# Kernel optimization log

Measured on AMD Instinct MI355X. Metric: run time of the kernel, lower is better.

The kernel has to match this reference:

```python
import jax, jax.numpy as jnp
import numpy as np

B, L, D, H = 2, 2048, 1024, 16
HD = D // H  # head_dim = 64


def _clin(xr, xi, Wr, br, Wi, bi):
    # (x_r + i x_i)(W_r + i W_i): out_r = fc_r(x_r) - fc_i(x_i); out_i = fc_r(x_i) + fc_i(x_r)
    rr = xr @ Wr.T + br
    ii = xi @ Wi.T + bi
    ri = xi @ Wr.T + br
    ir = xr @ Wi.T + bi
    return rr - ii, ri + ir


def _heads(x):
    # [B, L, D] -> [B, H, L, HD]
    return x.reshape(B, L, H, HD).transpose(0, 2, 1, 3)


def setup_inputs() -> dict:
    key = jax.random.key(0)
    ks = jax.random.split(key, 11)
    inp = {
        "x_r": jax.random.normal(ks[0], (B, L, D), jnp.float32),
        "x_i": jax.random.normal(ks[1], (B, L, D), jnp.float32),
        "attention_mask": jnp.zeros((B, 1, 1, L), jnp.float32),
    }
    names = ["Wq_r", "Wq_i", "Wk_r", "Wk_i", "Wv_r", "Wv_i", "Wo_r", "Wo_i"]
    for n, k in zip(names, ks[2:10]):
        inp[n] = jax.random.normal(k, (D, D), jnp.float32) * 0.02
        inp["b" + n[1:]] = jnp.zeros((D,), jnp.float32)
    return inp


def reference(x_r, x_i, attention_mask,
              Wq_r, bq_r, Wq_i, bq_i,
              Wk_r, bk_r, Wk_i, bk_i,
              Wv_r, bv_r, Wv_i, bv_i,
              Wo_r, bo_r, Wo_i, bo_i):
    qr, qi = _clin(x_r, x_i, Wq_r, bq_r, Wq_i, bq_i)
    kr, ki = _clin(x_r, x_i, Wk_r, bk_r, Wk_i, bk_i)
    vr, vi = _clin(x_r, x_i, Wv_r, bv_r, Wv_i, bv_i)
    q_r, q_i = _heads(qr), _heads(qi)
    k_r, k_i = _heads(kr), _heads(ki)
    v_r, v_i = _heads(vr), _heads(vi)
    # complex QK^T cross terms -> squared-magnitude interference score
    s_real = jnp.einsum('bhqd,bhkd->bhqk', q_r, k_r) + jnp.einsum('bhqd,bhkd->bhqk', q_i, k_i)
    s_imag = jnp.einsum('bhqd,bhkd->bhqk', q_i, k_r) - jnp.einsum('bhqd,bhkd->bhqk', q_r, k_i)
    interference = (s_real * s_real + s_imag * s_imag) / HD + attention_mask
    attn = jax.nn.softmax(interference, axis=-1)
    c_r = jnp.einsum('bhqk,bhkd->bhqd', attn, v_r).transpose(0, 2, 1, 3).reshape(B, L, D)
    c_i = jnp.einsum('bhqk,bhkd->bhqd', attn, v_i).transpose(0, 2, 1, 3).reshape(B, L, D)
    out_r, out_i = _clin(c_r, c_i, Wo_r, bo_r, Wo_i, bo_i)
    return out_r, out_i
```

## Files before the change

### kernel.cpp

```cpp
#include <hip/hip_runtime.h>
#include <hip/hip_bf16.h>

typedef unsigned short u16;
typedef __attribute__((ext_vector_type(8))) short bf16x8;
typedef __attribute__((ext_vector_type(8))) _Float16 f16x8;
typedef __attribute__((ext_vector_type(2))) _Float16 f16x2;
typedef __attribute__((ext_vector_type(8))) unsigned short u16x8;
typedef __attribute__((ext_vector_type(4))) float f32x4;
typedef __attribute__((ext_vector_type(16))) float f32x16;

__device__ __forceinline__ u16 f2b(float f) {
  _Float16 h = (_Float16)f;
  return __builtin_bit_cast(u16, h);
}

__device__ __forceinline__ f32x4 mfma16(bf16x8 a, bf16x8 b, f32x4 c) {
  return __builtin_amdgcn_mfma_f32_16x16x32_f16(
      __builtin_bit_cast(f16x8, a), __builtin_bit_cast(f16x8, b), c, 0, 0, 0);
}

__device__ __forceinline__ f32x16 mfma32(bf16x8 a, bf16x8 b, f32x16 c) {
  return __builtin_amdgcn_mfma_f32_32x32x16_f16(
      __builtin_bit_cast(f16x8, a), __builtin_bit_cast(f16x8, b), c, 0, 0, 0);
}

__device__ __forceinline__ float fexp2(float x) {
  float r; asm("v_exp_f32 %0, %1" : "=v"(r) : "v"(x)); return r;
}

#define GLD16(dst, src) __builtin_amdgcn_global_load_lds( \
    (const __attribute__((address_space(1))) void*)(src), \
    (__attribute__((address_space(3))) void*)(dst), 16, 0, 0)

__global__ void pack_x_kernel(u16* __restrict__ A1, const float* __restrict__ xr,
                              const float* __restrict__ xi) {
  const int id = blockIdx.x * 256 + threadIdx.x;
  const size_t k8 = (size_t)id * 8;
  const int n = (int)(k8 >> 11);
  const int kk = (int)(k8 & 2047);
  const float* src = (kk < 1024) ? (xr + (size_t)n * 1024 + kk)
                                 : (xi + (size_t)n * 1024 + (kk - 1024));
  float4 a = *(const float4*)src;
  float4 c = *(const float4*)(src + 4);
  u16x8 o;
  o[0] = f2b(a.x); o[1] = f2b(a.y); o[2] = f2b(a.z); o[3] = f2b(a.w);
  o[4] = f2b(c.x); o[5] = f2b(c.y); o[6] = f2b(c.z); o[7] = f2b(c.w);
  *(u16x8*)(A1 + k8) = o;
}

struct PWArgs {
  const float* Wr[4]; const float* Wi[4];
  const float* br[4]; const float* bi[4];
};

__global__ void pack_w_all(PWArgs a, int sbase, u16* __restrict__ B1,
                           u16* __restrict__ B2, float* __restrict__ bias1,
                           float* __restrict__ bias2) {
  const int s = sbase + blockIdx.y;
  const int wi = s >> 1, isim = s & 1;
  u16* dst = (s < 6) ? (B1 + (size_t)s * (1024 * 2048))
                     : (B2 + (size_t)(s - 6) * (1024 * 2048));
  float* biasDst = (s < 6) ? (bias1 + s * 1024) : (bias2 + (s - 6) * 1024);
  const int row = blockIdx.x;
  const int kk = threadIdx.x * 8;
  const int half = kk >> 10;
  const int kloc = kk & 1023;
  const float* W = (half == 0) ? (isim ? a.Wi[wi] : a.Wr[wi])
                               : (isim ? a.Wr[wi] : a.Wi[wi]);
  const float sgn = (half == 1 && !isim) ? -1.f : 1.f;
  const float* src = W + (size_t)row * 1024 + kloc;
  float4 x = *(const float4*)src;
  float4 c = *(const float4*)(src + 4);
  u16x8 o;
  o[0] = f2b(sgn * x.x); o[1] = f2b(sgn * x.y); o[2] = f2b(sgn * x.z); o[3] = f2b(sgn * x.w);
  o[4] = f2b(sgn * c.x); o[5] = f2b(sgn * c.y); o[6] = f2b(sgn * c.z); o[7] = f2b(sgn * c.w);
  *(u16x8*)(dst + (size_t)row * 2048 + kk) = o;
  if (threadIdx.x == 0)
    biasDst[row] = isim ? (a.br[wi][row] + a.bi[wi][row])
                        : (a.br[wi][row] - a.bi[wi][row]);
}

template<int MODE>
__global__ __launch_bounds__(256) void gemm_bt(const u16* __restrict__ A,
                                               const u16* __restrict__ Bw,
                                               const float* __restrict__ bias,
                                               void* __restrict__ outp,
                                               u16* __restrict__ vtp) {
  constexpr int K = 2048;
  __shared__ __align__(16) u16 As[128 * 64];
  __shared__ __align__(16) u16 Bs[128 * 64];
  const int tid = threadIdx.x;
  const int w = tid >> 6, l = tid & 63;
  const int l15 = l & 15, lhi = l >> 4;
  const int m0 = blockIdx.y * 128, n0 = blockIdx.x * 128;
  const int wm = w >> 1, wn = w & 1;
  f32x4 acc[4][4] = {};
  for (int kt = 0; kt < K; kt += 64) {
#pragma unroll
    for (int it = 0; it < 4; ++it) {
      const int grp = it * 4 + w;
      const int cl = grp * 64 + l;
      const int r = cl >> 3;
      const int g = (cl & 7) ^ (r & 7);
      GLD16(As + grp * 512, A + (size_t)(m0 + r) * K + kt + g * 8);
      GLD16(Bs + grp * 512, Bw + (size_t)(n0 + r) * K + kt + g * 8);
    }
    __syncthreads();
#pragma unroll
    for (int ks = 0; ks < 2; ++ks) {
      const int c = ks * 4 + lhi;
      bf16x8 af[4], bfr[4];
#pragma unroll
      for (int mf = 0; mf < 4; ++mf) {
        const int r = wm * 64 + mf * 16 + l15;
        af[mf] = *(const bf16x8*)&As[r * 64 + ((c ^ (r & 7)) << 3)];
      }
#pragma unroll
      for (int nf = 0; nf < 4; ++nf) {
        const int r = wn * 64 + nf * 16 + l15;
        bfr[nf] = *(const bf16x8*)&Bs[r * 64 + ((c ^ (r & 7)) << 3)];
      }
#pragma unroll
      for (int mf = 0; mf < 4; ++mf)
#pragma unroll
        for (int nf = 0; nf < 4; ++nf)
          acc[mf][nf] = mfma16(af[mf], bfr[nf], acc[mf][nf]);
    }
    __syncthreads();
  }
#pragma unroll
  for (int nf = 0; nf < 4; ++nf) {
    const int j = n0 + wn * 64 + nf * 16 + l15;
    const float bv = bias[j];
    if constexpr (MODE == 1) {
      const size_t obase = (size_t)(j >> 10) * (4096 * 1024) + (j & 1023);
#pragma unroll
      for (int mf = 0; mf < 4; ++mf)
#pragma unroll
        for (int i = 0; i < 4; ++i) {
          const int row = m0 + wm * 64 + mf * 16 + lhi * 4 + i;
          ((float*)outp)[obase + (size_t)row * 1024] = acc[mf][nf][i] + bv;
        }
    } else {
      if (j < 4096) {
        const size_t obase = (size_t)(j >> 10) * (4096 * 1024) + (j & 1023);
#pragma unroll
        for (int mf = 0; mf < 4; ++mf)
#pragma unroll
          for (int i = 0; i < 4; ++i) {
            const int row = m0 + wm * 64 + mf * 16 + lhi * 4 + i;
            ((u16*)outp)[obase + (size_t)row * 1024] = f2b(acc[mf][nf][i] + bv);
          }
      } else {
        const int jv = j - 4096;
        const size_t vb = (size_t)(jv >> 10) * 4194304 +
                          (size_t)((jv >> 6) & 15) * 131072 +
                          (size_t)(jv & 63) * 2048;
#pragma unroll
        for (int mf = 0; mf < 4; ++mf)
#pragma unroll
          for (int i = 0; i < 4; ++i) {
            const int row = m0 + wm * 64 + mf * 16 + lhi * 4 + i;
            const int b2 = row >> 11, tok = row & 2047;
            vtp[vb + (size_t)b2 * 2097152 + tok] = f2b(acc[mf][nf][i] + bv);
          }
      }
    }
  }
}

__global__ __launch_bounds__(256, 2) void attn_kernel(const u16* __restrict__ qkv,
                                                      const u16* __restrict__ vt,
                                                      const float* __restrict__ mask,
                                                      u16* __restrict__ A2) {
  __shared__ __align__(16) u16 KVb[2][4][2048];
  __shared__ float maskL[2048];
  const int tid = threadIdx.x, w = tid >> 6, l = tid & 63;
  const int tok = l & 31, hi = l >> 5;
  const int q0 = blockIdx.x * 128;
  const int bh = blockIdx.y;
  const int b = bh >> 4, h = bh & 15;
  const size_t M1 = (size_t)4096 * 1024;
  const u16* qr_b = qkv;
  const u16* qi_b = qkv + M1;
  const u16* kr_b = qkv + 2 * M1;
  const u16* ki_b = qkv + 3 * M1;
  const u16* vtr = vt;
  const u16* vti = vt + (size_t)32 * 64 * 2048;
  constexpr float LOG2E = 1.4426950408889634f;
  constexpr float C2 = 0.015625f * LOG2E;

  {
    const float4* msrc = (const float4*)(mask + (size_t)b * 2048);
    float4 m0 = msrc[tid * 2], m1 = msrc[tid * 2 + 1];
    float4 s0 = {m0.x * LOG2E, m0.y * LOG2E, m0.z * LOG2E, m0.w * LOG2E};
    float4 s1 = {m1.x * LOG2E, m1.y * LOG2E, m1.z * LOG2E, m1.w * LOG2E};
    *(float4*)&maskL[tid * 8] = s0;
    *(float4*)&maskL[tid * 8 + 4] = s1;
  }

  const size_t qrow = (size_t)(b * 2048 + q0 + w * 32 + tok) * 1024 + h * 64 + hi * 8;
  bf16x8 qr[4], qi[4], qrn[4];
#pragma unroll
  for (int ks = 0; ks < 4; ++ks) {
    qr[ks] = *(const bf16x8*)&qr_b[qrow + ks * 16];
    qi[ks] = *(const bf16x8*)&qi_b[qrow + ks * 16];
    qrn[ks] = qr[ks] ^ (short)0x8000;
  }
  float mrow = -1e30f, srow = 0.f;
  f32x16 o_r[2] = {}, o_i[2] = {};

  auto STAGE = [&](int tile, int bufi) {
    const int k0s = tile * 32;
    if (w < 2) {
      const u16* src = w ? ki_b : kr_b;
      u16* dstb = &KVb[bufi][w][0];
#pragma unroll
      for (int it = 0; it < 4; ++it) {
        const int cl = it * 64 + l;
        const int r = cl >> 3;
        const int g = (cl & 7) ^ (r & 7);
        GLD16(dstb + it * 512, src + (size_t)(b * 2048 + k0s + r) * 1024 + h * 64 + g * 8);
      }
    } else {
      const u16* src = (w == 3) ? vti : vtr;
      u16* dstb = &KVb[bufi][w][0];
#pragma unroll
      for (int it = 0; it < 4; ++it) {
        const int cl = it * 64 + l;
        const int r = cl >> 2;
        const int g = (cl & 3) ^ ((r >> 1) & 3);
        GLD16(dstb + it * 512, src + (size_t)(bh * 64 + r) * 2048 + k0s + g * 8);
      }
    }
  };

  const int krow = tok * 64;
  const int ksw = tok & 7;

  STAGE(0, 0);
#pragma unroll 2
  for (int kt = 0; kt < 64; ++kt) {
    const int cur = kt & 1;
    const int k0 = kt * 32;
    __syncthreads();
    if (kt < 63) STAGE(kt + 1, cur ^ 1);
    const u16* Kr = &KVb[cur][0][0];
    const u16* Ki = &KVb[cur][1][0];
    const u16* Vr = &KVb[cur][2][0];
    const u16* Vi = &KVb[cur][3][0];
    f32x16 sr = {}, si = {};
    __builtin_amdgcn_s_setprio(1);
#pragma unroll
    for (int ks = 0; ks < 4; ++ks) {
      const int off = krow + (((ks * 2 + hi) ^ ksw) << 3);
      bf16x8 kfr = *(const bf16x8*)&Kr[off];
      bf16x8 kfi = *(const bf16x8*)&Ki[off];
      sr = mfma32(kfr, qr[ks], sr);
      sr = mfma32(kfi, qi[ks], sr);
      si = mfma32(kfr, qi[ks], si);
      si = mfma32(kfi, qrn[ks], si);
    }
    __builtin_amdgcn_s_setprio(0);
    float t[16];
#pragma unroll
    for (int qd = 0; qd < 4; ++qd) {
      const float4 mk = *(const float4*)&maskL[k0 + qd * 8 + hi * 4];
#pragma unroll
      for (int j = 0; j < 4; ++j) {
        const int r = qd * 4 + j;
        const float ss = fmaf(si[r], si[r], sr[r] * sr[r]);
        t[r] = fmaf(ss, C2, ((const float*)&mk)[j]);
      }
    }
    float pmax = t[0];
#pragma unroll
    for (int r = 1; r < 16; ++r) pmax = fmaxf(pmax, t[r]);
    pmax = fmaxf(pmax, __shfl_xor(pmax, 32, 64));
    if (__any(pmax > mrow + 11.f)) {
      const float mn = fmaxf(mrow, pmax);
      const float sc = fexp2(mrow - mn);
      mrow = mn;
      srow *= sc;
#pragma unroll
      for (int r = 0; r < 16; ++r) {
        const float scr = __shfl(sc, (r & 3) + 8 * (r >> 2) + 4 * hi, 64);
        o_r[0][r] *= scr; o_r[1][r] *= scr;
        o_i[0][r] *= scr; o_i[1][r] *= scr;
      }
    }
    float p[16];
#pragma unroll
    for (int r = 0; r < 16; ++r) {
      p[r] = fexp2(t[r] - mrow);
      srow += p[r];
    }
    unsigned P[8];
#pragma unroll
    for (int e = 0; e < 8; ++e)
      P[e] = __builtin_bit_cast(unsigned,
               __builtin_amdgcn_cvt_pkrtz(p[2 * e], p[2 * e + 1]));
    const bool h0 = (hi == 0);
    const unsigned r0 = (unsigned)__shfl_xor((int)(h0 ? P[2] : P[0]), 32, 64);
    const unsigned r1 = (unsigned)__shfl_xor((int)(h0 ? P[3] : P[1]), 32, 64);
    const unsigned r2 = (unsigned)__shfl_xor((int)(h0 ? P[6] : P[4]), 32, 64);
    const unsigned r3 = (unsigned)__shfl_xor((int)(h0 ? P[7] : P[5]), 32, 64);
    unsigned fa0[4] = { h0 ? P[0] : r0, h0 ? P[1] : r1, h0 ? r0 : P[2], h0 ? r1 : P[3] };
    unsigned fa1[4] = { h0 ? P[4] : r2, h0 ? P[5] : r3, h0 ? r2 : P[6], h0 ? r3 : P[7] };
    bf16x8 pa0, pa1;
#pragma unroll
    for (int e = 0; e < 4; ++e) {
      ((unsigned*)&pa0)[e] = fa0[e];
      ((unsigned*)&pa1)[e] = fa1[e];
    }
    __builtin_amdgcn_s_setprio(1);
#pragma unroll
    for (int nf = 0; nf < 2; ++nf) {
      const int dv = nf * 32 + tok;
      const int vsw = (dv >> 1) & 3;
      const int voff0 = dv * 32 + ((hi ^ vsw) << 3);
      const int voff1 = dv * 32 + (((2 + hi) ^ vsw) << 3);
      o_r[nf] = mfma32(pa0, *(const bf16x8*)&Vr[voff0], o_r[nf]);
      o_i[nf] = mfma32(pa0, *(const bf16x8*)&Vi[voff0], o_i[nf]);
      o_r[nf] = mfma32(pa1, *(const bf16x8*)&Vr[voff1], o_r[nf]);
      o_i[nf] = mfma32(pa1, *(const bf16x8*)&Vi[voff1], o_i[nf]);
    }
    __builtin_amdgcn_s_setprio(0);
  }
  const float stot = srow + __shfl_xor(srow, 32, 64);
  const float invq = 1.f / stot;
  const int rowbase = b * 2048 + q0 + w * 32;
#pragma unroll
  for (int r = 0; r < 16; ++r) {
    const int qr2 = (r & 3) + 8 * (r >> 2) + 4 * hi;
    const float iv = __shfl(invq, qr2, 64);
    const size_t rw = (size_t)(rowbase + qr2) * 2048;
#pragma unroll
    for (int nf = 0; nf < 2; ++nf) {
      const int col = h * 64 + nf * 32 + tok;
      A2[rw + col] = f2b(o_r[nf][r] * iv);
      A2[rw + 1024 + col] = f2b(o_i[nf][r] * iv);
    }
  }
}

extern "C" void kernel_launch(void* const* d_in, const int* in_sizes, int n_in,
                              void* d_out, int out_size, void* d_ws, size_t ws_size,
                              hipStream_t stream) {
  (void)in_sizes; (void)n_in; (void)out_size; (void)ws_size;
  const float* x_r  = (const float*)d_in[0];
  const float* x_i  = (const float*)d_in[1];
  const float* mask = (const float*)d_in[2];

  PWArgs pw;
  pw.Wr[0] = (const float*)d_in[3];  pw.br[0] = (const float*)d_in[4];
  pw.Wi[0] = (const float*)d_in[5];  pw.bi[0] = (const float*)d_in[6];
  pw.Wr[1] = (const float*)d_in[7];  pw.br[1] = (const float*)d_in[8];
  pw.Wi[1] = (const float*)d_in[9];  pw.bi[1] = (const float*)d_in[10];
  pw.Wr[2] = (const float*)d_in[11]; pw.br[2] = (const float*)d_in[12];
  pw.Wi[2] = (const float*)d_in[13]; pw.bi[2] = (const float*)d_in[14];
  pw.Wr[3] = (const float*)d_in[15]; pw.br[3] = (const float*)d_in[16];
  pw.Wi[3] = (const float*)d_in[17]; pw.bi[3] = (const float*)d_in[18];

  char* ws = (char*)d_ws;
  u16* A     = (u16*)(ws);
  u16* B1    = (u16*)(ws + (16u << 20));
  u16* B2    = (u16*)(ws + (16u << 20));
  u16* qkvp  = (u16*)(ws + (40u << 20));
  u16* vtp   = (u16*)(ws + (72u << 20));
  float* bias1 = (float*)(ws + (88u << 20));
  float* bias2 = (float*)(ws + (88u << 20) + (1u << 15));

  pack_x_kernel<<<4096, 256, 0, stream>>>(A, x_r, x_i);
  pack_w_all<<<dim3(1024, 6), 256, 0, stream>>>(pw, 0, B1, B2, bias1, bias2);

  gemm_bt<0><<<dim3(48, 32), 256, 0, stream>>>(A, B1, bias1, qkvp, vtp);

  pack_w_all<<<dim3(1024, 2), 256, 0, stream>>>(pw, 6, B1, B2, bias1, bias2);

  attn_kernel<<<dim3(16, 32), 256, 0, stream>>>(qkvp, vtp, mask, A);

  gemm_bt<1><<<dim3(16, 32), 256, 0, stream>>>(A, B2, bias2, d_out, nullptr);
}
```

Before: 422.5 us.

## Double-buffer GEMM with 128x256 tiles, 8 waves, interleaved prefetch and block swizzle

Rewrites the projection GEMM as a 512-thread, 128x256-tile kernel with double-buffered LDS. Global loads for the next k-tiles are split into chunks issued between MFMA phases, using explicit vmcnt waits, barriers and setprio. This is meant to hide global memory latency behind the matrix math. Workgroup IDs are also swizzled in groups of 8 to improve cache locality. In exchange the kernel uses more LDS and adds fragile manual synchronization, and the grids shrink to fewer, larger blocks.

```diff
diff --git a/kernel.cpp b/kernel.cpp
--- a/kernel.cpp
+++ b/kernel.cpp
@@ -4,7 +4,6 @@
 typedef unsigned short u16;
 typedef __attribute__((ext_vector_type(8))) short bf16x8;
 typedef __attribute__((ext_vector_type(8))) _Float16 f16x8;
-typedef __attribute__((ext_vector_type(2))) _Float16 f16x2;
 typedef __attribute__((ext_vector_type(8))) unsigned short u16x8;
 typedef __attribute__((ext_vector_type(4))) float f32x4;
 typedef __attribute__((ext_vector_type(16))) float f32x16;
@@ -81,53 +80,117 @@
 }
 
 template<int MODE>
-__global__ __launch_bounds__(256) void gemm_bt(const u16* __restrict__ A,
+__global__ __launch_bounds__(512) void gemm_bt(const u16* __restrict__ A,
                                                const u16* __restrict__ Bw,
                                                const float* __restrict__ bias,
                                                void* __restrict__ outp,
                                                u16* __restrict__ vtp) {
   constexpr int K = 2048;
-  __shared__ __align__(16) u16 As[128 * 64];
-  __shared__ __align__(16) u16 Bs[128 * 64];
+  constexpr int NT = K / 64;
+  __shared__ __align__(16) u16 Ab[2][128 * 64];
+  __shared__ __align__(16) u16 Bb[2][256 * 64];
   const int tid = threadIdx.x;
   const int w = tid >> 6, l = tid & 63;
   const int l15 = l & 15, lhi = l >> 4;
-  const int m0 = blockIdx.y * 128, n0 = blockIdx.x * 128;
-  const int wm = w >> 1, wn = w & 1;
+  const int wm = w >> 2, wn = w & 3;
+  const int nwg = gridDim.x * gridDim.y;
+  const int orig = blockIdx.x + blockIdx.y * gridDim.x;
+  const int swz = (orig & 7) * (nwg >> 3) + (orig >> 3);
+  const int bx = swz % gridDim.x, by = swz / gridDim.x;
+  const int m0 = by * 128, n0 = bx * 256;
+
+  auto STG = [&](int t, int r) {
+    const int q = t & 1;
+    const int kt = t * 64;
+    const int row8 = w * 8 + (l >> 3);
+    const int g = (l & 7) ^ ((l >> 3) & 7);
+    if (r < 2)
+      GLD16(&Ab[q][r * 4096 + w * 512],
+            A + (size_t)(m0 + r * 64 + row8) * K + kt + g * 8);
+    else
+      GLD16(&Bb[q][(r - 2) * 4096 + w * 512],
+            Bw + (size_t)(n0 + (r - 2) * 64 + row8) * K + kt + g * 8);
+  };
+
   f32x4 acc[4][4] = {};
-  for (int kt = 0; kt < K; kt += 64) {
-#pragma unroll
-    for (int it = 0; it < 4; ++it) {
-      const int grp = it * 4 + w;
-      const int cl = grp * 64 + l;
-      const int r = cl >> 3;
-      const int g = (cl & 7) ^ (r & 7);
-      GLD16(As + grp * 512, A + (size_t)(m0 + r) * K + kt + g * 8);
-      GLD16(Bs + grp * 512, Bw + (size_t)(n0 + r) * K + kt + g * 8);
-    }
-    __syncthreads();
-#pragma unroll
-    for (int ks = 0; ks < 2; ++ks) {
-      const int c = ks * 4 + lhi;
-      bf16x8 af[4], bfr[4];
-#pragma unroll
-      for (int mf = 0; mf < 4; ++mf) {
-        const int r = wm * 64 + mf * 16 + l15;
-        af[mf] = *(const bf16x8*)&As[r * 64 + ((c ^ (r & 7)) << 3)];
-      }
-#pragma unroll
-      for (int nf = 0; nf < 4; ++nf) {
-        const int r = wn * 64 + nf * 16 + l15;
-        bfr[nf] = *(const bf16x8*)&Bs[r * 64 + ((c ^ (r & 7)) << 3)];
-      }
-#pragma unroll
-      for (int mf = 0; mf < 4; ++mf)
-#pragma unroll
-        for (int nf = 0; nf < 4; ++nf)
-          acc[mf][nf] = mfma16(af[mf], bfr[nf], acc[mf][nf]);
-    }
-    __syncthreads();
-  }
+
+#pragma unroll
+  for (int r = 0; r < 6; ++r) STG(0, r);
+#pragma unroll
+  for (int r = 0; r < 4; ++r) STG(1, r);
+  asm volatile("s_waitcnt vmcnt(4)" ::: "memory");
+  __builtin_amdgcn_sched_barrier(0);
+  __builtin_amdgcn_s_barrier();
+
+  for (int t = 0; t < NT; ++t) {
+    const int q = t & 1;
+    const u16* Aq = &Ab[q][0];
+    const u16* Bq = &Bb[q][0];
+    bf16x8 a0[4], b0[4], a1[4], b1[4];
+#pragma unroll
+    for (int mf = 0; mf < 4; ++mf) {
+      const int r = wm * 64 + mf * 16 + l15;
+      a0[mf] = *(const bf16x8*)&Aq[r * 64 + ((lhi ^ (r & 7)) << 3)];
+    }
+#pragma unroll
+    for (int nf = 0; nf < 4; ++nf) {
+      const int r = wn * 64 + nf * 16 + l15;
+      b0[nf] = *(const bf16x8*)&Bq[r * 64 + ((lhi ^ (r & 7)) << 3)];
+    }
+    if (t + 1 < NT) { STG(t + 1, 4); STG(t + 1, 5); }
+    __builtin_amdgcn_s_barrier();
+    __builtin_amdgcn_s_setprio(1);
+#pragma unroll
+    for (int mf = 0; mf < 2; ++mf)
+#pragma unroll
+      for (int nf = 0; nf < 4; ++nf)
+        acc[mf][nf] = mfma16(a0[mf], b0[nf], acc[mf][nf]);
+    __builtin_amdgcn_s_setprio(0);
+    __builtin_amdgcn_s_barrier();
+#pragma unroll
+    for (int mf = 0; mf < 4; ++mf) {
+      const int r = wm * 64 + mf * 16 + l15;
+      a1[mf] = *(const bf16x8*)&Aq[r * 64 + (((4 + lhi) ^ (r & 7)) << 3)];
+    }
+#pragma unroll
+    for (int nf = 0; nf < 4; ++nf) {
+      const int r = wn * 64 + nf * 16 + l15;
+      b1[nf] = *(const bf16x8*)&Bq[r * 64 + (((4 + lhi) ^ (r & 7)) << 3)];
+    }
+    __builtin_amdgcn_sched_barrier(0);
+    __builtin_amdgcn_s_barrier();
+    __builtin_amdgcn_s_setprio(1);
+#pragma unroll
+    for (int mf = 2; mf < 4; ++mf)
+#pragma unroll
+      for (int nf = 0; nf < 4; ++nf)
+        acc[mf][nf] = mfma16(a0[mf], b0[nf], acc[mf][nf]);
+    __builtin_amdgcn_s_setprio(0);
+    __builtin_amdgcn_s_barrier();
+    if (t + 2 < NT) { STG(t + 2, 0); STG(t + 2, 1); }
+    __builtin_amdgcn_s_barrier();
+    __builtin_amdgcn_s_setprio(1);
+#pragma unroll
+    for (int mf = 0; mf < 2; ++mf)
+#pragma unroll
+      for (int nf = 0; nf < 4; ++nf)
+        acc[mf][nf] = mfma16(a1[mf], b1[nf], acc[mf][nf]);
+    __builtin_amdgcn_s_setprio(0);
+    __builtin_amdgcn_s_barrier();
+    if (t + 2 < NT) { STG(t + 2, 2); STG(t + 2, 3); }
+    __builtin_amdgcn_s_setprio(1);
+#pragma unroll
+    for (int mf = 2; mf < 4; ++mf)
+#pragma unroll
+      for (int nf = 0; nf < 4; ++nf)
+        acc[mf][nf] = mfma16(a1[mf], b1[nf], acc[mf][nf]);
+    __builtin_amdgcn_s_setprio(0);
+    if (t < NT - 2) { asm volatile("s_waitcnt vmcnt(4)" ::: "memory"); }
+    else            { asm volatile("s_waitcnt vmcnt(0)" ::: "memory"); }
+    __builtin_amdgcn_sched_barrier(0);
+    __builtin_amdgcn_s_barrier();
+  }
+
 #pragma unroll
   for (int nf = 0; nf < 4; ++nf) {
     const int j = n0 + wn * 64 + nf * 16 + l15;
@@ -374,11 +437,11 @@
   pack_x_kernel<<<4096, 256, 0, stream>>>(A, x_r, x_i);
   pack_w_all<<<dim3(1024, 6), 256, 0, stream>>>(pw, 0, B1, B2, bias1, bias2);
 
-  gemm_bt<0><<<dim3(48, 32), 256, 0, stream>>>(A, B1, bias1, qkvp, vtp);
+  gemm_bt<0><<<dim3(24, 32), 512, 0, stream>>>(A, B1, bias1, qkvp, vtp);
 
   pack_w_all<<<dim3(1024, 2), 256, 0, stream>>>(pw, 6, B1, B2, bias1, bias2);
 
   attn_kernel<<<dim3(16, 32), 256, 0, stream>>>(qkvp, vtp, mask, A);
 
-  gemm_bt<1><<<dim3(16, 32), 256, 0, stream>>>(A, B2, bias2, d_out, nullptr);
-}
+  gemm_bt<1><<<dim3(8, 32), 512, 0, stream>>>(A, B2, bias2, d_out, nullptr);
+}
```

Measured after the change: 434.2 us. 1.03x slower.

## Pipeline GEMM with triple-buffered async loads and wider 128x256 tiles

Applied to the files above, without the earlier changes.

Reworks the projection GEMM to use a three-stage LDS ring buffer with BK=32. Loads for stage t+2 are issued while stage t computes, and a single barrier per iteration is gated by vmcnt waits. Each block now covers a 128x256 output tile, with every wave owning a full 128x64 slab, and MFMA issue priority is raised. This targets global-load latency stalls and the double barrier per k-step. The cost is more accumulator registers, 2-blocks-per-CU launch bounds, and half as many blocks in the grid, which may hurt occupancy and wave balance.

```diff
diff --git a/kernel.cpp b/kernel.cpp
--- a/kernel.cpp
+++ b/kernel.cpp
@@ -4,7 +4,6 @@
 typedef unsigned short u16;
 typedef __attribute__((ext_vector_type(8))) short bf16x8;
 typedef __attribute__((ext_vector_type(8))) _Float16 f16x8;
-typedef __attribute__((ext_vector_type(2))) _Float16 f16x2;
 typedef __attribute__((ext_vector_type(8))) unsigned short u16x8;
 typedef __attribute__((ext_vector_type(4))) float f32x4;
 typedef __attribute__((ext_vector_type(16))) float f32x16;
@@ -81,74 +80,95 @@
 }
 
 template<int MODE>
-__global__ __launch_bounds__(256) void gemm_bt(const u16* __restrict__ A,
-                                               const u16* __restrict__ Bw,
-                                               const float* __restrict__ bias,
-                                               void* __restrict__ outp,
-                                               u16* __restrict__ vtp) {
+__global__ __launch_bounds__(256, 2) void gemm_bt(const u16* __restrict__ A,
+                                                  const u16* __restrict__ Bw,
+                                                  const float* __restrict__ bias,
+                                                  void* __restrict__ outp,
+                                                  u16* __restrict__ vtp) {
   constexpr int K = 2048;
-  __shared__ __align__(16) u16 As[128 * 64];
-  __shared__ __align__(16) u16 Bs[128 * 64];
+  constexpr int NT = 64;
+  __shared__ __align__(16) u16 Ab[3][128 * 32];
+  __shared__ __align__(16) u16 Bb[3][256 * 32];
   const int tid = threadIdx.x;
   const int w = tid >> 6, l = tid & 63;
   const int l15 = l & 15, lhi = l >> 4;
-  const int m0 = blockIdx.y * 128, n0 = blockIdx.x * 128;
-  const int wm = w >> 1, wn = w & 1;
-  f32x4 acc[4][4] = {};
-  for (int kt = 0; kt < K; kt += 64) {
-#pragma unroll
-    for (int it = 0; it < 4; ++it) {
-      const int grp = it * 4 + w;
-      const int cl = grp * 64 + l;
-      const int r = cl >> 3;
-      const int g = (cl & 7) ^ (r & 7);
-      GLD16(As + grp * 512, A + (size_t)(m0 + r) * K + kt + g * 8);
-      GLD16(Bs + grp * 512, Bw + (size_t)(n0 + r) * K + kt + g * 8);
-    }
-    __syncthreads();
-#pragma unroll
-    for (int ks = 0; ks < 2; ++ks) {
-      const int c = ks * 4 + lhi;
-      bf16x8 af[4], bfr[4];
-#pragma unroll
-      for (int mf = 0; mf < 4; ++mf) {
-        const int r = wm * 64 + mf * 16 + l15;
-        af[mf] = *(const bf16x8*)&As[r * 64 + ((c ^ (r & 7)) << 3)];
-      }
-#pragma unroll
-      for (int nf = 0; nf < 4; ++nf) {
-        const int r = wn * 64 + nf * 16 + l15;
-        bfr[nf] = *(const bf16x8*)&Bs[r * 64 + ((c ^ (r & 7)) << 3)];
-      }
-#pragma unroll
-      for (int mf = 0; mf < 4; ++mf)
-#pragma unroll
-        for (int nf = 0; nf < 4; ++nf)
-          acc[mf][nf] = mfma16(af[mf], bfr[nf], acc[mf][nf]);
-    }
-    __syncthreads();
-  }
+  const int m0 = blockIdx.y * 128, n0 = blockIdx.x * 256;
+
+  auto STG = [&](int t) {
+    const int sl = t % 3;
+    const int kt = t * 32;
+#pragma unroll
+    for (int r = 0; r < 2; ++r) {
+      const int c = r * 256 + tid;
+      const int row = c >> 2;
+      const int g = (c & 3) ^ ((row >> 1) & 3);
+      GLD16(&Ab[sl][(r * 256 + w * 64) * 8],
+            A + (size_t)(m0 + row) * K + kt + g * 8);
+    }
+#pragma unroll
+    for (int r = 0; r < 4; ++r) {
+      const int c = r * 256 + tid;
+      const int row = c >> 2;
+      const int g = (c & 3) ^ ((row >> 1) & 3);
+      GLD16(&Bb[sl][(r * 256 + w * 64) * 8],
+            Bw + (size_t)(n0 + row) * K + kt + g * 8);
+    }
+  };
+
+  f32x4 acc[8][4] = {};
+
+  STG(0); STG(1);
+  for (int t = 0; t < NT; ++t) {
+    if (t < NT - 1) { asm volatile("s_waitcnt vmcnt(6)" ::: "memory"); }
+    else            { asm volatile("s_waitcnt vmcnt(0)" ::: "memory"); }
+    __builtin_amdgcn_sched_barrier(0);
+    __builtin_amdgcn_s_barrier();
+    __builtin_amdgcn_sched_barrier(0);
+    if (t + 2 < NT) STG(t + 2);
+    const int sl = t % 3;
+    const u16* Aq = &Ab[sl][0];
+    const u16* Bq = &Bb[sl][0];
+    bf16x8 af[8], bfr[4];
+#pragma unroll
+    for (int mf = 0; mf < 8; ++mf) {
+      const int rr = mf * 16 + l15;
+      af[mf] = *(const bf16x8*)&Aq[rr * 32 + ((lhi ^ ((rr >> 1) & 3)) << 3)];
+    }
+#pragma unroll
+    for (int nf = 0; nf < 4; ++nf) {
+      const int rr = w * 64 + nf * 16 + l15;
+      bfr[nf] = *(const bf16x8*)&Bq[rr * 32 + ((lhi ^ ((rr >> 1) & 3)) << 3)];
+    }
+    __builtin_amdgcn_s_setprio(1);
+#pragma unroll
+    for (int mf = 0; mf < 8; ++mf)
+#pragma unroll
+      for (int nf = 0; nf < 4; ++nf)
+        acc[mf][nf] = mfma16(af[mf], bfr[nf], acc[mf][nf]);
+    __builtin_amdgcn_s_setprio(0);
+  }
+
 #pragma unroll
   for (int nf = 0; nf < 4; ++nf) {
-    const int j = n0 + wn * 64 + nf * 16 + l15;
+    const int j = n0 + w * 64 + nf * 16 + l15;
     const float bv = bias[j];
     if constexpr (MODE == 1) {
       const size_t obase = (size_t)(j >> 10) * (4096 * 1024) + (j & 1023);
 #pragma unroll
-      for (int mf = 0; mf < 4; ++mf)
+      for (int mf = 0; mf < 8; ++mf)
 #pragma unroll
         for (int i = 0; i < 4; ++i) {
-          const int row = m0 + wm * 64 + mf * 16 + lhi * 4 + i;
+          const int row = m0 + mf * 16 + lhi * 4 + i;
           ((float*)outp)[obase + (size_t)row * 1024] = acc[mf][nf][i] + bv;
         }
     } else {
       if (j < 4096) {
         const size_t obase = (size_t)(j >> 10) * (4096 * 1024) + (j & 1023);
 #pragma unroll
-        for (int mf = 0; mf < 4; ++mf)
+        for (int mf = 0; mf < 8; ++mf)
 #pragma unroll
           for (int i = 0; i < 4; ++i) {
-            const int row = m0 + wm * 64 + mf * 16 + lhi * 4 + i;
+            const int row = m0 + mf * 16 + lhi * 4 + i;
             ((u16*)outp)[obase + (size_t)row * 1024] = f2b(acc[mf][nf][i] + bv);
           }
       } else {
@@ -157,10 +177,10 @@
                           (size_t)((jv >> 6) & 15) * 131072 +
                           (size_t)(jv & 63) * 2048;
 #pragma unroll
-        for (int mf = 0; mf < 4; ++mf)
+        for (int mf = 0; mf < 8; ++mf)
 #pragma unroll
           for (int i = 0; i < 4; ++i) {
-            const int row = m0 + wm * 64 + mf * 16 + lhi * 4 + i;
+            const int row = m0 + mf * 16 + lhi * 4 + i;
             const int b2 = row >> 11, tok = row & 2047;
             vtp[vb + (size_t)b2 * 2097152 + tok] = f2b(acc[mf][nf][i] + bv);
           }
@@ -374,11 +394,11 @@
   pack_x_kernel<<<4096, 256, 0, stream>>>(A, x_r, x_i);
   pack_w_all<<<dim3(1024, 6), 256, 0, stream>>>(pw, 0, B1, B2, bias1, bias2);
 
-  gemm_bt<0><<<dim3(48, 32), 256, 0, stream>>>(A, B1, bias1, qkvp, vtp);
+  gemm_bt<0><<<dim3(24, 32), 256, 0, stream>>>(A, B1, bias1, qkvp, vtp);
 
   pack_w_all<<<dim3(1024, 2), 256, 0, stream>>>(pw, 6, B1, B2, bias1, bias2);
 
   attn_kernel<<<dim3(16, 32), 256, 0, stream>>>(qkvp, vtp, mask, A);
 
-  gemm_bt<1><<<dim3(16, 32), 256, 0, stream>>>(A, B2, bias2, d_out, nullptr);
-}
+  gemm_bt<1><<<dim3(8, 32), 256, 0, stream>>>(A, B2, bias2, d_out, nullptr);
+}
```

After: 483.2 us. +14.4%, slower.

## Triple-buffer GEMM LDS tiles with async prefetch and 128x256 block tiles

Applied to the files above, without the earlier changes.

Rewrites the projection GEMM to use 512-thread blocks computing 128x256 tiles. Global-to-LDS loads are spread over a three-stage ring with a two-tile prefetch distance, gated by explicit vmcnt waits and raw s_barrier calls instead of __syncthreads. MFMA sections are raised to higher wave priority to overlap loads with compute. This cuts grid size in half and uses far more LDS per block, which forces one block per CU and lowers occupancy.

```diff
diff --git a/kernel.cpp b/kernel.cpp
--- a/kernel.cpp
+++ b/kernel.cpp
@@ -4,7 +4,6 @@
 typedef unsigned short u16;
 typedef __attribute__((ext_vector_type(8))) short bf16x8;
 typedef __attribute__((ext_vector_type(8))) _Float16 f16x8;
-typedef __attribute__((ext_vector_type(2))) _Float16 f16x2;
 typedef __attribute__((ext_vector_type(8))) unsigned short u16x8;
 typedef __attribute__((ext_vector_type(4))) float f32x4;
 typedef __attribute__((ext_vector_type(16))) float f32x16;
@@ -81,53 +80,75 @@
 }
 
 template<int MODE>
-__global__ __launch_bounds__(256) void gemm_bt(const u16* __restrict__ A,
-                                               const u16* __restrict__ Bw,
-                                               const float* __restrict__ bias,
-                                               void* __restrict__ outp,
-                                               u16* __restrict__ vtp) {
+__global__ __launch_bounds__(512, 1) void gemm_bt(const u16* __restrict__ A,
+                                                  const u16* __restrict__ Bw,
+                                                  const float* __restrict__ bias,
+                                                  void* __restrict__ outp,
+                                                  u16* __restrict__ vtp) {
   constexpr int K = 2048;
-  __shared__ __align__(16) u16 As[128 * 64];
-  __shared__ __align__(16) u16 Bs[128 * 64];
+  constexpr int NT = 32;
+  __shared__ __align__(16) u16 Ab[3][128 * 64];
+  __shared__ __align__(16) u16 Bb[3][256 * 64];
   const int tid = threadIdx.x;
   const int w = tid >> 6, l = tid & 63;
   const int l15 = l & 15, lhi = l >> 4;
-  const int m0 = blockIdx.y * 128, n0 = blockIdx.x * 128;
-  const int wm = w >> 1, wn = w & 1;
+  const int wm = w >> 2, wn = w & 3;
+  const int m0 = blockIdx.y * 128, n0 = blockIdx.x * 256;
+
+  const int row8 = w * 8 + (l >> 3);
+  const int g8 = (l & 7) ^ ((l >> 3) & 7);
+  auto STG = [&](int t) {
+    const int sl = t % 3;
+    const int kt = t * 64;
+#pragma unroll
+    for (int r = 0; r < 2; ++r)
+      GLD16(&Ab[sl][r * 4096 + w * 512],
+            A + (size_t)(m0 + r * 64 + row8) * K + kt + g8 * 8);
+#pragma unroll
+    for (int r = 0; r < 4; ++r)
+      GLD16(&Bb[sl][r * 4096 + w * 512],
+            Bw + (size_t)(n0 + r * 64 + row8) * K + kt + g8 * 8);
+  };
+
   f32x4 acc[4][4] = {};
-  for (int kt = 0; kt < K; kt += 64) {
-#pragma unroll
-    for (int it = 0; it < 4; ++it) {
-      const int grp = it * 4 + w;
-      const int cl = grp * 64 + l;
-      const int r = cl >> 3;
-      const int g = (cl & 7) ^ (r & 7);
-      GLD16(As + grp * 512, A + (size_t)(m0 + r) * K + kt + g * 8);
-      GLD16(Bs + grp * 512, Bw + (size_t)(n0 + r) * K + kt + g * 8);
-    }
-    __syncthreads();
+
+  STG(0); STG(1);
+  for (int t = 0; t < NT; ++t) {
+    if (t + 2 < NT) { asm volatile("s_waitcnt vmcnt(6)" ::: "memory"); }
+    else            { asm volatile("s_waitcnt vmcnt(0)" ::: "memory"); }
+    __builtin_amdgcn_sched_barrier(0);
+    __builtin_amdgcn_s_barrier();
+    if (t + 2 < NT) STG(t + 2);
+    const int sl = t % 3;
+    const u16* Aq = &Ab[sl][0];
+    const u16* Bq = &Bb[sl][0];
 #pragma unroll
     for (int ks = 0; ks < 2; ++ks) {
       const int c = ks * 4 + lhi;
       bf16x8 af[4], bfr[4];
 #pragma unroll
       for (int mf = 0; mf < 4; ++mf) {
-        const int r = wm * 64 + mf * 16 + l15;
-        af[mf] = *(const bf16x8*)&As[r * 64 + ((c ^ (r & 7)) << 3)];
+        const int rr = wm * 64 + mf * 16 + l15;
+        af[mf] = *(const bf16x8*)&Aq[rr * 64 + ((c ^ (rr & 7)) << 3)];
       }
 #pragma unroll
       for (int nf = 0; nf < 4; ++nf) {
-        const int r = wn * 64 + nf * 16 + l15;
-        bfr[nf] = *(const bf16x8*)&Bs[r * 64 + ((c ^ (r & 7)) << 3)];
-      }
+        const int rr = wn * 64 + nf * 16 + l15;
+        bfr[nf] = *(const bf16x8*)&Bq[rr * 64 + ((c ^ (rr & 7)) << 3)];
+      }
+      asm volatile("s_waitcnt lgkmcnt(0)" ::: "memory");
+      __builtin_amdgcn_sched_barrier(0);
+      __builtin_amdgcn_s_setprio(1);
 #pragma unroll
       for (int mf = 0; mf < 4; ++mf)
 #pragma unroll
         for (int nf = 0; nf < 4; ++nf)
           acc[mf][nf] = mfma16(af[mf], bfr[nf], acc[mf][nf]);
-    }
-    __syncthreads();
-  }
+      __builtin_amdgcn_s_setprio(0);
+      __builtin_amdgcn_s_barrier();
+    }
+  }
+
 #pragma unroll
   for (int nf = 0; nf < 4; ++nf) {
     const int j = n0 + wn * 64 + nf * 16 + l15;
@@ -374,11 +395,11 @@
   pack_x_kernel<<<4096, 256, 0, stream>>>(A, x_r, x_i);
   pack_w_all<<<dim3(1024, 6), 256, 0, stream>>>(pw, 0, B1, B2, bias1, bias2);
 
-  gemm_bt<0><<<dim3(48, 32), 256, 0, stream>>>(A, B1, bias1, qkvp, vtp);
+  gemm_bt<0><<<dim3(24, 32), 512, 0, stream>>>(A, B1, bias1, qkvp, vtp);
 
   pack_w_all<<<dim3(1024, 2), 256, 0, stream>>>(pw, 6, B1, B2, bias1, bias2);
 
   attn_kernel<<<dim3(16, 32), 256, 0, stream>>>(qkvp, vtp, mask, A);
 
-  gemm_bt<1><<<dim3(16, 32), 256, 0, stream>>>(A, B2, bias2, d_out, nullptr);
-}
+  gemm_bt<1><<<dim3(8, 32), 512, 0, stream>>>(A, B2, bias2, d_out, nullptr);
+}
```

Measured after the change: 460.9 us. 9.1% more time.
